# Optimization experiments

Measured on AMD Instinct MI355X. Metric: run time of the kernel, lower is better.

The kernel has to match this reference:

```python
import jax, jax.numpy as jnp
import numpy as np

N_USERS, N_MOVIES, H, E = 100000, 50000, 128, 1000000


def setup_inputs() -> dict:
    key = jax.random.key(0)
    k1, k2, k3, k4, k5, k6 = jax.random.split(key, 6)
    scale1 = 1.0 / np.sqrt(2 * H)  # torch Linear default-ish init scale
    scale2 = 1.0 / np.sqrt(H)
    return {
        "z_user": jax.random.normal(k1, (N_USERS, H), dtype=jnp.float32),
        "z_movie": jax.random.normal(k2, (N_MOVIES, H), dtype=jnp.float32),
        "row": jax.random.randint(k3, (E,), 0, N_USERS, dtype=jnp.int64) if jax.config.jax_enable_x64 else jax.random.randint(k3, (E,), 0, N_USERS, dtype=jnp.int32),
        "col": jax.random.randint(k4, (E,), 0, N_MOVIES, dtype=jnp.int32),
        "W1": jax.random.normal(k5, (H, 2 * H), dtype=jnp.float32) * scale1,
        "b1": jnp.zeros((H,), dtype=jnp.float32),
        "W2": jax.random.normal(k6, (1, H), dtype=jnp.float32) * scale2,
        "b2": jnp.zeros((1,), dtype=jnp.float32),
    }


def reference(z_user, z_movie, row, col, W1, b1, W2, b2):
    zu = z_user[row]            # [E, H] gather
    zm = z_movie[col]           # [E, H] gather
    z = jnp.concatenate([zu, zm], axis=-1)        # [E, 2H]
    h = jax.nn.relu(z @ W1.T + b1)                # [E, H]
    out = h @ W2.T + b2                           # [E, 1]
    return out.reshape(-1)
```

## Files before the change

### kernel.cpp

```cpp
#include <hip/hip_runtime.h>
#include <stdint.h>

typedef __attribute__((ext_vector_type(8))) short bf16x8;
typedef __attribute__((ext_vector_type(8))) char  char8;
typedef __attribute__((ext_vector_type(4))) float f32x4;
typedef __attribute__((ext_vector_type(4))) int   i32x4;

#define SU      (4.5f / 127.0f)
#define INV_SU  (127.0f / 4.5f)

__device__ __forceinline__ unsigned short f2bf(float f) {
    uint32_t u = __builtin_bit_cast(uint32_t, f);
    uint32_t r = (u + 0x7FFFu + ((u >> 16) & 1u)) >> 16;
    return (unsigned short)r;
}

__device__ __forceinline__ bf16x8 cvt8(f32x4 a, f32x4 b) {
    bf16x8 v;
#pragma unroll
    for (int i = 0; i < 4; ++i) v[i] = (short)f2bf(a[i]);
#pragma unroll
    for (int i = 0; i < 4; ++i) v[4 + i] = (short)f2bf(b[i]);
    return v;
}

__global__ void w1cvt(const float* __restrict__ W1, unsigned short* __restrict__ w1bf) {
    const int idx  = blockIdx.x * 256 + threadIdx.x;
    const int half = idx >> 11;
    const int rem  = idx & 2047;
    const int nt   = rem >> 8;
    const int ks   = (rem >> 6) & 3;
    const int lane = rem & 63;
    const int lm   = lane & 15;
    const int g    = lane >> 4;
    const float* src = W1 + (nt * 16 + lm) * 256 + half * 128 + ks * 32 + g * 8;
    f32x4 a = *reinterpret_cast<const f32x4*>(src);
    f32x4 b = *reinterpret_cast<const f32x4*>(src + 4);
    *reinterpret_cast<bf16x8*>(w1bf + (size_t)idx * 8) = cvt8(a, b);
}

__global__ __launch_bounds__(256) void precompute_h1(
    const float* __restrict__ zu, const float* __restrict__ zm,
    const unsigned short* __restrict__ w1bf, const float* __restrict__ b1,
    char* __restrict__ h1u8, char* __restrict__ h1m8,
    int Mu, int Mm, int bu)
{
    const int tid  = threadIdx.x;
    const int wid  = tid >> 6;
    const int lane = tid & 63;
    const int g    = lane >> 4;
    const int lm   = lane & 15;

    const bool isU = (int)blockIdx.x < bu;
    const float* z = isU ? zu : zm;
    char* h1       = isU ? h1u8 : h1m8;
    const int M    = isU ? Mu : Mm;
    const unsigned short* wb = w1bf + (isU ? 0 : (size_t)2048 * 8);
    const int rbase = (isU ? blockIdx.x : blockIdx.x - bu) * 128 + wid * 32;

    f32x4 acc[2][8];
#pragma unroll
    for (int mt = 0; mt < 2; ++mt)
#pragma unroll
        for (int nt = 0; nt < 8; ++nt) acc[mt][nt] = f32x4{0.f, 0.f, 0.f, 0.f};

#pragma unroll
    for (int ks = 0; ks < 4; ++ks) {
        bf16x8 a[2];
#pragma unroll
        for (int mt = 0; mt < 2; ++mt) {
            int r = rbase + mt * 16 + lm;
            r = r < M ? r : M - 1;
            const float* p = z + (size_t)r * 128 + ks * 32 + g * 8;
            f32x4 x0 = *reinterpret_cast<const f32x4*>(p);
            f32x4 x1 = *reinterpret_cast<const f32x4*>(p + 4);
            a[mt] = cvt8(x0, x1);
        }
#pragma unroll
        for (int nt = 0; nt < 8; ++nt) {
            bf16x8 bfr = *reinterpret_cast<const bf16x8*>(
                wb + ((size_t)(nt * 4 + ks) * 64 + lane) * 8);
#pragma unroll
            for (int mt = 0; mt < 2; ++mt)
                acc[mt][nt] = __builtin_amdgcn_mfma_f32_16x16x32_bf16(
                    bfr, a[mt], acc[mt][nt], 0, 0, 0);
        }
    }

    f32x4 b1q[8];
#pragma unroll
    for (int nt = 0; nt < 8; ++nt) {
        f32x4 t = *reinterpret_cast<const f32x4*>(b1 + nt * 16 + g * 4);
#pragma unroll
        for (int r = 0; r < 4; ++r) b1q[nt][r] = 0.5f * t[r];
    }

#pragma unroll
    for (int mt = 0; mt < 2; ++mt) {
        const int m = rbase + mt * 16 + lm;
        if (m >= M) continue;
#pragma unroll
        for (int nt = 0; nt < 8; ++nt) {
            uint32_t p = 0;
#pragma unroll
            for (int r = 0; r < 4; ++r) {
                float h  = acc[mt][nt][r] + b1q[nt][r];
                float qf = fmaxf(-127.f, fminf(127.f, __builtin_rintf(h * INV_SU)));
                int   q  = (int)qf;
                p |= (uint32_t)(q & 0xff) << (8 * r);
            }
            *reinterpret_cast<uint32_t*>(h1 + (size_t)m * 128 + nt * 16 + g * 4) = p;
        }
    }
}

__global__ __launch_bounds__(256) void edge_score(
    const char* __restrict__ h1u8, const char* __restrict__ h1m8,
    const int* __restrict__ row, const int* __restrict__ col,
    const float* __restrict__ W2, const float* __restrict__ b2,
    float* __restrict__ out, int nE)
{
    const int tid = blockIdx.x * 256 + threadIdx.x;
    const int g   = tid >> 4;
    const int l   = tid & 15;
    const int e0  = g * 8;
    if (e0 >= nE) return;

    float w2s[8];
    {
        f32x4 c0 = *reinterpret_cast<const f32x4*>(W2 + l * 8);
        f32x4 c1 = *reinterpret_cast<const f32x4*>(W2 + l * 8 + 4);
#pragma unroll
        for (int j = 0; j < 4; ++j) { w2s[j] = c0[j] * SU; w2s[4 + j] = c1[j] * SU; }
    }
    const float b2s = b2[0];

    int ridx[8], cidx[8];
    if (e0 + 8 <= nE) {
        i32x4 r0 = __builtin_nontemporal_load(reinterpret_cast<const i32x4*>(row + e0));
        i32x4 r1 = __builtin_nontemporal_load(reinterpret_cast<const i32x4*>(row + e0 + 4));
        i32x4 c0 = __builtin_nontemporal_load(reinterpret_cast<const i32x4*>(col + e0));
        i32x4 c1 = __builtin_nontemporal_load(reinterpret_cast<const i32x4*>(col + e0 + 4));
#pragma unroll
        for (int j = 0; j < 4; ++j) { ridx[j] = r0[j]; ridx[4 + j] = r1[j]; }
#pragma unroll
        for (int j = 0; j < 4; ++j) { cidx[j] = c0[j]; cidx[4 + j] = c1[j]; }
    } else {
#pragma unroll
        for (int j = 0; j < 8; ++j) {
            int e = e0 + j;
            e = e < nE ? e : nE - 1;
            ridx[j] = row[e];
            cidx[j] = col[e];
        }
    }

    char8 u[8], m[8];
#pragma unroll
    for (int j = 0; j < 8; ++j)
        u[j] = *reinterpret_cast<const char8*>(h1u8 + (size_t)ridx[j] * 128 + l * 8);
#pragma unroll
    for (int j = 0; j < 8; ++j)
        m[j] = *reinterpret_cast<const char8*>(h1m8 + (size_t)cidx[j] * 128 + l * 8);
    __builtin_amdgcn_sched_barrier(0);

    float s[8];
#pragma unroll
    for (int j = 0; j < 8; ++j) {
        float acc = 0.f;
#pragma unroll
        for (int q = 0; q < 8; ++q) {
            int su = (int)u[j][q] + (int)m[j][q];
            su = su > 0 ? su : 0;
            acc = fmaf((float)su, w2s[q], acc);
        }
        acc += __shfl_xor(acc, 1);
        acc += __shfl_xor(acc, 2);
        acc += __shfl_xor(acc, 4);
        acc += __shfl_xor(acc, 8);
        s[j] = acc + b2s;
    }

    float v = 0.f;
#pragma unroll
    for (int j = 0; j < 8; ++j) v = (l == j) ? s[j] : v;
    const int e = e0 + l;
    if (l < 8 && e < nE) __builtin_nontemporal_store(v, out + e);
}

__device__ __forceinline__ unsigned swzB(int n, int kbyte) {
    return ((unsigned)(n * 512 + kbyte)) ^ (unsigned)((n & 7) << 4);
}

__global__ __launch_bounds__(256, 2) void edge_mlp_fallback(
    const float* __restrict__ z_user, const float* __restrict__ z_movie,
    const int* __restrict__ row, const int* __restrict__ col,
    const float* __restrict__ W1, const float* __restrict__ b1,
    const float* __restrict__ W2, const float* __restrict__ b2,
    float* __restrict__ out, int nE, int ntiles)
{
    __shared__ __align__(16) char Bs[65536];
    const int tid  = threadIdx.x;
    const int wid  = tid >> 6;
    const int lane = tid & 63;
    const int g    = lane >> 4;
    const int lm   = lane & 15;

#pragma unroll
    for (int it = 0; it < 16; ++it) {
        int c  = it * 256 + tid;
        int n  = c >> 5;
        int kc = c & 31;
        const float* src = W1 + n * 256 + kc * 8;
        f32x4 a = *reinterpret_cast<const f32x4*>(src);
        f32x4 b = *reinterpret_cast<const f32x4*>(src + 4);
        *reinterpret_cast<bf16x8*>(&Bs[swzB(n, kc * 16)]) = cvt8(a, b);
    }
    __syncthreads();

    float b1v[8], w2v[8];
#pragma unroll
    for (int nt = 0; nt < 8; ++nt) {
        int n = nt * 16 + lm;
        b1v[nt] = b1[n];
        w2v[nt] = W2[n];
    }
    const float b2s = b2[0];

    for (int tile = blockIdx.x; tile < ntiles; tile += gridDim.x) {
        const int ebase = tile * 256 + wid * 64;
        int re[4], ce[4];
#pragma unroll
        for (int mt = 0; mt < 4; ++mt) {
            int e = ebase + mt * 16 + lm;
            e = e < nE ? e : nE - 1;
            re[mt] = row[e];
            ce[mt] = col[e];
        }
        f32x4 acc[4][8];
#pragma unroll
        for (int mt = 0; mt < 4; ++mt)
#pragma unroll
            for (int nt = 0; nt < 8; ++nt) acc[mt][nt] = f32x4{0.f, 0.f, 0.f, 0.f};
#pragma unroll
        for (int half = 0; half < 2; ++half) {
#pragma unroll
            for (int ks = 0; ks < 4; ++ks) {
                bf16x8 a[4];
#pragma unroll
                for (int mt = 0; mt < 4; ++mt) {
                    const float* p = (half ? z_movie + (size_t)ce[mt] * 128
                                           : z_user + (size_t)re[mt] * 128) + ks * 32 + g * 8;
                    f32x4 x0 = *reinterpret_cast<const f32x4*>(p);
                    f32x4 x1 = *reinterpret_cast<const f32x4*>(p + 4);
                    a[mt] = cvt8(x0, x1);
                }
                const int kbyte = (half * 128 + ks * 32 + g * 8) * 2;
#pragma unroll
                for (int nt = 0; nt < 8; ++nt) {
                    bf16x8 bfr = *reinterpret_cast<const bf16x8*>(&Bs[swzB(nt * 16 + lm, kbyte)]);
#pragma unroll
                    for (int mt = 0; mt < 4; ++mt)
                        acc[mt][nt] = __builtin_amdgcn_mfma_f32_16x16x32_bf16(
                            a[mt], bfr, acc[mt][nt], 0, 0, 0);
                }
            }
        }
#pragma unroll
        for (int mt = 0; mt < 4; ++mt) {
#pragma unroll
            for (int r = 0; r < 4; ++r) {
                float s = 0.f;
#pragma unroll
                for (int nt = 0; nt < 8; ++nt)
                    s += fmaxf(acc[mt][nt][r] + b1v[nt], 0.f) * w2v[nt];
                s += __shfl_xor(s, 8);
                s += __shfl_xor(s, 4);
                s += __shfl_xor(s, 2);
                s += __shfl_xor(s, 1);
                if (lm == 0) {
                    int e = ebase + mt * 16 + g * 4 + r;
                    if (e < nE) out[e] = s + b2s;
                }
            }
        }
    }
}

extern "C" void kernel_launch(void* const* d_in, const int* in_sizes, int n_in,
                              void* d_out, int out_size, void* d_ws, size_t ws_size,
                              hipStream_t stream) {
    const float* z_user  = (const float*)d_in[0];
    const float* z_movie = (const float*)d_in[1];
    const int*   row     = (const int*)d_in[2];
    const int*   col     = (const int*)d_in[3];
    const float* W1      = (const float*)d_in[4];
    const float* b1      = (const float*)d_in[5];
    const float* W2      = (const float*)d_in[6];
    const float* b2      = (const float*)d_in[7];
    float*       out     = (float*)d_out;

    const int nE = in_sizes[2];
    const int Mu = in_sizes[0] / 128;
    const int Mm = in_sizes[1] / 128;

    const size_t tblBytes = ((size_t)Mu + (size_t)Mm) * 128;
    const size_t need     = tblBytes + 65536;

    if (ws_size >= need) {
        char* h1u8 = (char*)d_ws;
        char* h1m8 = h1u8 + (size_t)Mu * 128;
        unsigned short* w1bf = (unsigned short*)(h1u8 + tblBytes);

        w1cvt<<<16, 256, 0, stream>>>(W1, w1bf);

        const int bu = (Mu + 127) / 128;
        const int bm = (Mm + 127) / 128;
        precompute_h1<<<bu + bm, 256, 0, stream>>>(z_user, z_movie, w1bf, b1,
                                                   h1u8, h1m8, Mu, Mm, bu);

        const int nGroups = (nE + 7) / 8;
        const int blocks  = (nGroups * 16 + 255) / 256;
        edge_score<<<blocks, 256, 0, stream>>>(h1u8, h1m8, row, col,
                                               W2, b2, out, nE);
    } else {
        const int ntiles = (nE + 255) / 256;
        const int grid   = ntiles < 512 ? ntiles : 512;
        edge_mlp_fallback<<<grid, 256, 0, stream>>>(z_user, z_movie, row, col,
                                                    W1, b1, W2, b2, out, nE, ntiles);
    }
}
```

Measured before the change: 71.80 us.

## Stage precompute_h1 input and int8 output through double-buffered LDS with coalesced access

```diff
diff --git a/kernel.cpp b/kernel.cpp
--- a/kernel.cpp
+++ b/kernel.cpp
@@ -8,6 +8,9 @@
 
 #define SU      (4.5f / 127.0f)
 #define INV_SU  (127.0f / 4.5f)
+#define MAGIC   12582912.0f
+#define ZSTR    80
+#define HSTR    132
 
 __device__ __forceinline__ unsigned short f2bf(float f) {
     uint32_t u = __builtin_bit_cast(uint32_t, f);
@@ -45,6 +48,9 @@
     char* __restrict__ h1u8, char* __restrict__ h1m8,
     int Mu, int Mm, int bu)
 {
+    __shared__ __align__(16) char Zs[2][128 * ZSTR];
+    char* Hs = &Zs[0][0];
+
     const int tid  = threadIdx.x;
     const int wid  = tid >> 6;
     const int lane = tid & 63;
@@ -56,7 +62,25 @@
     char* h1       = isU ? h1u8 : h1m8;
     const int M    = isU ? Mu : Mm;
     const unsigned short* wb = w1bf + (isU ? 0 : (size_t)2048 * 8);
-    const int rbase = (isU ? blockIdx.x : blockIdx.x - bu) * 128 + wid * 32;
+    const int rbase0 = (isU ? blockIdx.x : blockIdx.x - bu) * 128;
+
+    const int srow = tid >> 1;
+    const int part = tid & 1;
+    int grow = rbase0 + srow;
+    grow = grow < M ? grow : M - 1;
+    const float* zrow = z + (size_t)grow * 128 + part * 16;
+
+    {
+        const float* p = zrow;
+        f32x4 x0 = *reinterpret_cast<const f32x4*>(p);
+        f32x4 x1 = *reinterpret_cast<const f32x4*>(p + 4);
+        f32x4 x2 = *reinterpret_cast<const f32x4*>(p + 8);
+        f32x4 x3 = *reinterpret_cast<const f32x4*>(p + 12);
+        bf16x8* d = reinterpret_cast<bf16x8*>(&Zs[0][srow * ZSTR + part * 32]);
+        d[0] = cvt8(x0, x1);
+        d[1] = cvt8(x2, x3);
+    }
+    __syncthreads();
 
     f32x4 acc[2][8];
 #pragma unroll
@@ -65,26 +89,34 @@
         for (int nt = 0; nt < 8; ++nt) acc[mt][nt] = f32x4{0.f, 0.f, 0.f, 0.f};
 
 #pragma unroll
-    for (int ks = 0; ks < 4; ++ks) {
-        bf16x8 a[2];
-#pragma unroll
-        for (int mt = 0; mt < 2; ++mt) {
-            int r = rbase + mt * 16 + lm;
-            r = r < M ? r : M - 1;
-            const float* p = z + (size_t)r * 128 + ks * 32 + g * 8;
+    for (int s = 0; s < 4; ++s) {
+        if (s < 3) {
+            const float* p = zrow + (s + 1) * 32;
             f32x4 x0 = *reinterpret_cast<const f32x4*>(p);
             f32x4 x1 = *reinterpret_cast<const f32x4*>(p + 4);
-            a[mt] = cvt8(x0, x1);
-        }
+            f32x4 x2 = *reinterpret_cast<const f32x4*>(p + 8);
+            f32x4 x3 = *reinterpret_cast<const f32x4*>(p + 12);
+            bf16x8* d = reinterpret_cast<bf16x8*>(&Zs[(s + 1) & 1][srow * ZSTR + part * 32]);
+            d[0] = cvt8(x0, x1);
+            d[1] = cvt8(x2, x3);
+        }
+
+        bf16x8 a[2];
+#pragma unroll
+        for (int mt = 0; mt < 2; ++mt)
+            a[mt] = *reinterpret_cast<const bf16x8*>(
+                &Zs[s & 1][(wid * 32 + mt * 16 + lm) * ZSTR + g * 16]);
+
 #pragma unroll
         for (int nt = 0; nt < 8; ++nt) {
             bf16x8 bfr = *reinterpret_cast<const bf16x8*>(
-                wb + ((size_t)(nt * 4 + ks) * 64 + lane) * 8);
+                wb + ((size_t)(nt * 4 + s) * 64 + lane) * 8);
 #pragma unroll
             for (int mt = 0; mt < 2; ++mt)
                 acc[mt][nt] = __builtin_amdgcn_mfma_f32_16x16x32_bf16(
                     bfr, a[mt], acc[mt][nt], 0, 0, 0);
         }
+        __syncthreads();
     }
 
     f32x4 b1q[8];
@@ -92,24 +124,36 @@
     for (int nt = 0; nt < 8; ++nt) {
         f32x4 t = *reinterpret_cast<const f32x4*>(b1 + nt * 16 + g * 4);
 #pragma unroll
-        for (int r = 0; r < 4; ++r) b1q[nt][r] = 0.5f * t[r];
+        for (int r = 0; r < 4; ++r) b1q[nt][r] = 0.5f * INV_SU * t[r];
     }
 
 #pragma unroll
     for (int mt = 0; mt < 2; ++mt) {
-        const int m = rbase + mt * 16 + lm;
-        if (m >= M) continue;
+        const int mloc = wid * 32 + mt * 16 + lm;
 #pragma unroll
         for (int nt = 0; nt < 8; ++nt) {
             uint32_t p = 0;
 #pragma unroll
             for (int r = 0; r < 4; ++r) {
-                float h  = acc[mt][nt][r] + b1q[nt][r];
-                float qf = fmaxf(-127.f, fminf(127.f, __builtin_rintf(h * INV_SU)));
-                int   q  = (int)qf;
-                p |= (uint32_t)(q & 0xff) << (8 * r);
+                float t = fmaf(acc[mt][nt][r], INV_SU, b1q[nt][r]);
+                float c = fminf(127.f, fmaxf(-127.f, t));
+                float f = c + MAGIC;
+                p |= (__builtin_bit_cast(uint32_t, f) & 0xFFu) << (8 * r);
             }
-            *reinterpret_cast<uint32_t*>(h1 + (size_t)m * 128 + nt * 16 + g * 4) = p;
+            *reinterpret_cast<uint32_t*>(&Hs[mloc * HSTR + nt * 16 + g * 4]) = p;
+        }
+    }
+    __syncthreads();
+
+#pragma unroll
+    for (int i = 0; i < 4; ++i) {
+        const int c    = i * 256 + tid;
+        const int mloc = c >> 3;
+        const int off  = (c & 7) * 16;
+        const int m    = rbase0 + mloc;
+        if (m < M) {
+            i32x4 v = *reinterpret_cast<const i32x4*>(&Hs[mloc * HSTR + off]);
+            *reinterpret_cast<i32x4*>(h1 + (size_t)m * 128 + off) = v;
         }
     }
 }
```

Measured after the change: 73.47 us. 1.02x slower.
